# Performance work log

Measured on AMD Instinct MI355X. Metric: run time of the kernel, lower is better.

Reference implementation:

```python
import jax, jax.numpy as jnp
import numpy as np

# dims: B batch, CIN/COUT channels, K kernel, H/W spatial, S stride, P padding
B, CIN, COUT, K, H, W, S, P = 8, 16, 64, 3, 32, 32, 1, 1
ALPHA, R, N_EKV, VT, VD = 0.05625, 0.1, 1.5, 0.025, 0.1


def setup_inputs() -> dict:
    key = jax.random.key(0)
    k1, k2 = jax.random.split(key)
    x = jax.random.normal(k1, (B, CIN, H, W), dtype=jnp.float32)
    # torch init: uniform_(theta, 1.0, 8.0)
    theta = jax.random.uniform(k2, (COUT, CIN * K * K), dtype=jnp.float32, minval=1.0, maxval=8.0)
    scale = jnp.array(1.0, dtype=jnp.float32)
    return {"x": x, "theta": theta, "scale": scale}


def _unfold(x, k, s, p):
    # torch.nn.Unfold: patches flattened channel-major as (C, kh, kw)
    b, c, h, w = x.shape
    ho = (h + 2 * p - k) // s + 1
    wo = (w + 2 * p - k) // s + 1
    xp = jnp.pad(x, ((0, 0), (0, 0), (p, p), (p, p)))
    patches = jnp.stack(
        [xp[:, :, i:i + ho * s:s, j:j + wo * s:s] for i in range(k) for j in range(k)],
        axis=2,
    )  # (B, C, K*K, Ho, Wo)
    return patches.reshape(b, c * k * k, ho * wo), ho, wo


def _log1p_exp_stable_sq(a):
    # clamp to [-50, 20] then softplus; squared (EKV f)
    a = jnp.clip(a, -50.0, 20.0)
    sp = jnp.log1p(jnp.exp(a))
    return sp * sp


def reference(x, theta, scale):
    theta = jnp.clip(theta, 1.0, 8.0)  # mirrors theta.data.clamp_(1, 8)
    vg, ho, wo = _unfold(x, K, S, P)          # (B, Cin*K^2, L)
    vg = vg[:, None, :, :]                    # (B, 1, Cin*K^2, L)
    vth = theta[None, :, :, None]             # (1, Cout, Cin*K^2, 1)
    denom = 2.0 * N_EKV * VT
    term1 = _log1p_exp_stable_sq((vg - vth) / denom)
    term2 = _log1p_exp_stable_sq((vg - vth - VD) / denom)
    currents = jnp.clip(ALPHA * (term1 - term2), 0.0, None)
    i_k = jnp.sum(currents, axis=2)           # reduce over Cin*K^2 -> (B, Cout, L)
    v_out = i_k * R * scale
    return v_out.reshape(x.shape[0], COUT, ho, wo)
```

## Files before the change

### kernel.cpp

```cpp
#include <hip/hip_runtime.h>

#define BB 8
#define CIN 16
#define COUT 64
#define HH 32
#define WW 32
#define PH 34
#define PW 34
#define PPLANE (PH * PW)

#define SCALE_C 19.235933878519388f
#define K2E 0.26359713811472845f
#define B_HI 28.85390081777927f
#define WINLO_S (-13.849872392533959f)
#define OUT_CONST (0.4804530139182014f * 0.05625f * 0.1f)

#define EXP2F(x) __builtin_amdgcn_exp2f(x)
#define LOG2F(x) __builtin_amdgcn_logf(x)

#define NTH (COUT * CIN * 9)

__global__ __launch_bounds__(256) void init_kernel(const float* __restrict__ x,
                                                   const float* __restrict__ theta,
                                                   float* __restrict__ xp,
                                                   float* __restrict__ thp) {
    if (blockIdx.x < 578) {
        int idx = blockIdx.x * 256 + threadIdx.x;
        int c = idx / PPLANE;
        int r = idx - c * PPLANE;
        int y = r / PW;
        int xc = r - y * PW;
        float v = 0.0f;
        if (y >= 1 && y <= HH && xc >= 1 && xc <= WW) {
            v = x[c * (HH * WW) + (y - 1) * WW + (xc - 1)] * SCALE_C;
        }
        xp[idx] = v;
    } else {
        int i = (blockIdx.x - 578) * 256 + threadIdx.x;
        if (i < NTH) {
            thp[i] = fminf(fmaxf(theta[i], 1.0f), 8.0f) * SCALE_C;
        }
    }
}

__device__ __forceinline__ void load9(const float* __restrict__ p, float* v) {
#pragma unroll
    for (int dy = 0; dy < 3; ++dy)
#pragma unroll
        for (int dx = 0; dx < 3; ++dx)
            v[dy * 3 + dx] = p[dy * PW + dx];
}

__device__ __forceinline__ void compute9(const float* v, const float* __restrict__ thp,
                                         float* acc) {
#pragma unroll
    for (int k = 0; k < 9; ++k) {
        float b1 = v[k] - thp[k];
        if (__any(b1 > WINLO_S)) {
            float e1 = EXP2F(b1);
            float e2 = e1 * K2E;
            float l1 = fminf(LOG2F(1.0f + e1), B_HI);
            float l2 = fminf(LOG2F(1.0f + e2), B_HI);
            float a = acc[k % 3];
            a = fmaf(l1, l1, a);
            a = fmaf(-l2, l2, a);
            acc[k % 3] = a;
        }
    }
}

__global__ __launch_bounds__(256, 8) void ekv_kernel(const float* __restrict__ xp,
                                                     const float* __restrict__ thp,
                                                     const float* __restrict__ scale,
                                                     float* __restrict__ out) {
    int bid = blockIdx.x;
    int b = bid & 7;
    int tile = (bid >> 3) & 3;
    int cl = (bid >> 5) & 7;
    int cm = bid >> 8;
    int co = cm * 8 + cl;

    int t = threadIdx.x;
    int ow = t & 31;
    int oh = tile * 8 + (t >> 5);

    const float* thc = thp + co * (CIN * 9);
    const float* p0 = xp + (size_t)b * (CIN * PPLANE) + oh * PW + ow;

    float acc[3] = {0.0f, 0.0f, 0.0f};

    float va[9], vb[9];
    load9(p0, va);
#pragma unroll 1
    for (int cin = 0; cin < CIN; cin += 2) {
        load9(p0 + (cin + 1) * PPLANE, vb);
        compute9(va, thc + cin * 9, acc);
        int nc = cin + 2 < CIN ? cin + 2 : CIN - 1;
        load9(p0 + nc * PPLANE, va);
        compute9(vb, thc + (cin + 1) * 9, acc);
    }

    float sc = scale[0] * (OUT_CONST);
    out[(((size_t)b * COUT + co) * HH + oh) * WW + ow] =
        (acc[0] + acc[1] + acc[2]) * sc;
}

extern "C" void kernel_launch(void* const* d_in, const int* in_sizes, int n_in,
                              void* d_out, int out_size, void* d_ws, size_t ws_size,
                              hipStream_t stream) {
    const float* x = (const float*)d_in[0];
    const float* theta = (const float*)d_in[1];
    const float* scale = (const float*)d_in[2];
    float* out = (float*)d_out;

    float* thp = (float*)d_ws;
    float* xp = thp + NTH;
    (void)ws_size;

    init_kernel<<<578 + (NTH + 255) / 256, 256, 0, stream>>>(x, theta, xp, thp);
    ekv_kernel<<<BB * 4 * COUT, 256, 0, stream>>>(xp, thp, scale, out);
}
```

Baseline: 74.45 us.

## Fuse padding/prescale into main kernel via LDS-staged input tiles

Drops the separate init kernel that built a padded, prescaled copy of x and a clamped, prescaled theta. The EKV kernel now stages each block's halo tile (10x34 rows per channel, 8 channels per phase, two phases) into shared memory, applying padding and scaling on the fly. Per-output-channel theta is clamped into shared memory and read as float4. This removes one launch and a global round-trip, at the cost of redundant staging across the 64 output channels, extra barriers, and more LDS per block, which may reduce occupancy.

```diff
diff --git a/kernel.cpp b/kernel.cpp
--- a/kernel.cpp
+++ b/kernel.cpp
@@ -5,9 +5,6 @@
 #define COUT 64
 #define HH 32
 #define WW 32
-#define PH 34
-#define PW 34
-#define PPLANE (PH * PW)
 
 #define SCALE_C 19.235933878519388f
 #define K2E 0.26359713811472845f
@@ -18,44 +15,19 @@
 #define EXP2F(x) __builtin_amdgcn_exp2f(x)
 #define LOG2F(x) __builtin_amdgcn_logf(x)
 
-#define NTH (COUT * CIN * 9)
+#define XROWS 10
+#define XCOLS 34
+#define XPLANE (XROWS * XCOLS)
+#define PHASE_CINS 8
+#define STAGE_ELEMS (PHASE_CINS * XPLANE)
 
-__global__ __launch_bounds__(256) void init_kernel(const float* __restrict__ x,
-                                                   const float* __restrict__ theta,
-                                                   float* __restrict__ xp,
-                                                   float* __restrict__ thp) {
-    if (blockIdx.x < 578) {
-        int idx = blockIdx.x * 256 + threadIdx.x;
-        int c = idx / PPLANE;
-        int r = idx - c * PPLANE;
-        int y = r / PW;
-        int xc = r - y * PW;
-        float v = 0.0f;
-        if (y >= 1 && y <= HH && xc >= 1 && xc <= WW) {
-            v = x[c * (HH * WW) + (y - 1) * WW + (xc - 1)] * SCALE_C;
-        }
-        xp[idx] = v;
-    } else {
-        int i = (blockIdx.x - 578) * 256 + threadIdx.x;
-        if (i < NTH) {
-            thp[i] = fminf(fmaxf(theta[i], 1.0f), 8.0f) * SCALE_C;
-        }
-    }
-}
-
-__device__ __forceinline__ void load9(const float* __restrict__ p, float* v) {
-#pragma unroll
-    for (int dy = 0; dy < 3; ++dy)
-#pragma unroll
-        for (int dx = 0; dx < 3; ++dx)
-            v[dy * 3 + dx] = p[dy * PW + dx];
-}
-
-__device__ __forceinline__ void compute9(const float* v, const float* __restrict__ thp,
-                                         float* acc) {
+__device__ __forceinline__ void compute9(const float* v, const float4* th03,
+                                         const float4* th47, float th8, float* acc) {
+    float th[9] = {th03->x, th03->y, th03->z, th03->w,
+                   th47->x, th47->y, th47->z, th47->w, th8};
 #pragma unroll
     for (int k = 0; k < 9; ++k) {
-        float b1 = v[k] - thp[k];
+        float b1 = v[k] - th[k];
         if (__any(b1 > WINLO_S)) {
             float e1 = EXP2F(b1);
             float e2 = e1 * K2E;
@@ -69,38 +41,97 @@
     }
 }
 
-__global__ __launch_bounds__(256, 8) void ekv_kernel(const float* __restrict__ xp,
-                                                     const float* __restrict__ thp,
+__global__ __launch_bounds__(256, 8) void ekv_kernel(const float* __restrict__ x,
+                                                     const float* __restrict__ theta,
                                                      const float* __restrict__ scale,
                                                      float* __restrict__ out) {
     int bid = blockIdx.x;
     int b = bid & 7;
     int tile = (bid >> 3) & 3;
-    int cl = (bid >> 5) & 7;
-    int cm = bid >> 8;
-    int co = cm * 8 + cl;
+    int co = (bid >> 8) * 8 + ((bid >> 5) & 7);
 
     int t = threadIdx.x;
     int ow = t & 31;
-    int oh = tile * 8 + (t >> 5);
+    int ohl = t >> 5;
+    int oh = tile * 8 + ohl;
 
-    const float* thc = thp + co * (CIN * 9);
-    const float* p0 = xp + (size_t)b * (CIN * PPLANE) + oh * PW + ow;
+    __shared__ __align__(16) float s_x[STAGE_ELEMS];
+    __shared__ __align__(16) float s_th[CIN * 12];
 
-    float acc[3] = {0.0f, 0.0f, 0.0f};
-
-    float va[9], vb[9];
-    load9(p0, va);
-#pragma unroll 1
-    for (int cin = 0; cin < CIN; cin += 2) {
-        load9(p0 + (cin + 1) * PPLANE, vb);
-        compute9(va, thc + cin * 9, acc);
-        int nc = cin + 2 < CIN ? cin + 2 : CIN - 1;
-        load9(p0 + nc * PPLANE, va);
-        compute9(vb, thc + (cin + 1) * 9, acc);
+    if (t < CIN * 12) {
+        int cin = t / 12;
+        int j = t - cin * 12;
+        float v = 0.0f;
+        if (j < 9) v = fminf(fmaxf(theta[co * (CIN * 9) + cin * 9 + j], 1.0f), 8.0f) * SCALE_C;
+        s_th[t] = v;
     }
 
+    const float* xb = x + (size_t)b * (CIN * HH * WW);
+    float acc[3] = {0.0f, 0.0f, 0.0f};
     float sc = scale[0] * (OUT_CONST);
+
+    int pixbase = ohl * XCOLS + ow;
+
+#pragma unroll 1
+    for (int phase = 0; phase < 2; ++phase) {
+        int cinBase = phase * PHASE_CINS;
+        if (phase) __syncthreads();
+
+#pragma unroll 1
+        for (int i = t; i < STAGE_ELEMS; i += 256) {
+            int cinL = i / XPLANE;
+            int rem = i - cinL * XPLANE;
+            int r = rem / XCOLS;
+            int c = rem - r * XCOLS;
+            int gy = tile * 8 + r - 1;
+            int gx = c - 1;
+            float v = 0.0f;
+            if ((unsigned)gy < HH && (unsigned)gx < WW)
+                v = xb[((cinBase + cinL) * HH + gy) * WW + gx] * SCALE_C;
+            s_x[i] = v;
+        }
+        __syncthreads();
+
+        float va[9], vb[9];
+        {
+            const float* p = s_x + pixbase;
+#pragma unroll
+            for (int dy = 0; dy < 3; ++dy)
+#pragma unroll
+                for (int dx = 0; dx < 3; ++dx) va[dy * 3 + dx] = p[dy * XCOLS + dx];
+        }
+#pragma unroll 1
+        for (int cl = 0; cl < PHASE_CINS; cl += 2) {
+            {
+                const float* p = s_x + (cl + 1) * XPLANE + pixbase;
+#pragma unroll
+                for (int dy = 0; dy < 3; ++dy)
+#pragma unroll
+                    for (int dx = 0; dx < 3; ++dx) vb[dy * 3 + dx] = p[dy * XCOLS + dx];
+            }
+            {
+                int cin = cinBase + cl;
+                const float4* th03 = (const float4*)&s_th[cin * 12];
+                const float4* th47 = th03 + 1;
+                compute9(va, th03, th47, s_th[cin * 12 + 8], acc);
+            }
+            {
+                int nc = cl + 2 < PHASE_CINS ? cl + 2 : PHASE_CINS - 1;
+                const float* p = s_x + nc * XPLANE + pixbase;
+#pragma unroll
+                for (int dy = 0; dy < 3; ++dy)
+#pragma unroll
+                    for (int dx = 0; dx < 3; ++dx) va[dy * 3 + dx] = p[dy * XCOLS + dx];
+            }
+            {
+                int cin = cinBase + cl + 1;
+                const float4* th03 = (const float4*)&s_th[cin * 12];
+                const float4* th47 = th03 + 1;
+                compute9(vb, th03, th47, s_th[cin * 12 + 8], acc);
+            }
+        }
+    }
+
     out[(((size_t)b * COUT + co) * HH + oh) * WW + ow] =
         (acc[0] + acc[1] + acc[2]) * sc;
 }
@@ -112,11 +143,7 @@
     const float* theta = (const float*)d_in[1];
     const float* scale = (const float*)d_in[2];
     float* out = (float*)d_out;
+    (void)d_ws; (void)ws_size; (void)in_sizes; (void)n_in; (void)out_size;
 
-    float* thp = (float*)d_ws;
-    float* xp = thp + NTH;
-    (void)ws_size;
-
-    init_kernel<<<578 + (NTH + 255) / 256, 256, 0, stream>>>(x, theta, xp, thp);
-    ekv_kernel<<<BB * 4 * COUT, 256, 0, stream>>>(xp, thp, scale, out);
+    ekv_kernel<<<BB * 4 * COUT, 256, 0, stream>>>(x, theta, scale, out);
 }
```

New measurement: 78.63 us. 5.6% more time.
